# Kernel optimization log

Hardware: AMD Instinct MI355X
Metric: run time of the kernel (lower is better)

Reference implementation:

```python
import jax, jax.numpy as jnp
import numpy as np

# pywt db2 decomposition filters
DEC_LO = np.array([-0.12940952255092145, 0.22414386804185735,
                   0.836516303737469, 0.48296291314469025], dtype=np.float32)
DEC_HI = np.array([-0.48296291314469025, 0.836516303737469,
                   -0.22414386804185735, -0.12940952255092145], dtype=np.float32)

# pywt WaveletPacket2D.get_level(2, order='freq') graycode order over per-axis
# band paths: ['ll','lh','hh','hl'] -> (band at level1, band at level2), 0=low,1=high
GRAY = [(0, 0), (0, 1), (1, 1), (1, 0)]


def _pdwt_last(x, filts):
    """Single-level periodization-mode DWT along last axis.
    pywt 'per' mode (even N): out[i] = sum_j f[j] * x[(2i+1-j) mod N].
    Equivalent to circular left-pad by L-2 then VALID strided conv with the
    time-reversed filter. filts: [2, L] already reversed (lo, hi).
    Returns [..., 2, N//2] (band axis inserted before halved axis)."""
    *lead, N = x.shape
    L = filts.shape[-1]
    xe = jnp.concatenate([x[..., N - (L - 2):], x], axis=-1)  # [..., N+L-2]
    y = jax.lax.conv_general_dilated(
        xe.reshape(-1, 1, N + L - 2), filts[:, None, :],
        window_strides=(2,), padding='VALID')  # [B, 2, N//2]
    return y.reshape(*lead, 2, N // 2)


def _dwt2(x, filts):
    """2D single-level periodized DWT on the last two axes.
    x: [..., H, W] -> [..., 2(row band), 2(col band), H/2, W/2].
    Row band 1 = high-pass along axis -2 (pywt 'h' node = cH = 'da')."""
    y = _pdwt_last(x.swapaxes(-1, -2), filts)      # [..., W, 2, H/2]
    y = jnp.moveaxis(y, -2, -3).swapaxes(-1, -2)   # [..., 2, H/2, W]
    z = _pdwt_last(y, filts)                       # [..., 2, H/2, 2, W/2]
    return jnp.moveaxis(z, -2, -3)                 # [..., 2, 2, H/2, W/2]


def setup_inputs() -> dict:
    key = jax.random.key(0)
    x = jax.random.uniform(key, (3, 2048, 2048), dtype=jnp.float32)  # CHW in [0,1]
    return {"x": x, "dec_lo": jnp.asarray(DEC_LO), "dec_hi": jnp.asarray(DEC_HI)}


def reference(x, dec_lo, dec_hi):
    filts = jnp.stack([dec_lo[::-1], dec_hi[::-1]])  # time-reversed lo/hi, [2, L]
    b1 = _dwt2(x, filts)    # [C, 2, 2, H/2, W/2]            (r1, c1)
    b2 = _dwt2(b1, filts)   # [C, 2, 2, 2, 2, H/4, W/4]      (r1, c1, r2, c2)
    C = x.shape[0]
    h, w = b2.shape[-2:]
    # frequency-ordered 4x4 grid, flattened row-major, channels outermost
    bands = [b2[:, r1, c1, r2, c2] for (r1, r2) in GRAY for (c1, c2) in GRAY]
    y = jnp.stack(bands, axis=1)  # [C, 16, H/4, W/4]
    return y.reshape(C * 16, h, w)
```

## Files before the change

### kernel.cpp

```cpp
#include <hip/hip_runtime.h>

#define HH 2048
#define WW 2048
#define CC 3
#define OH 512
#define OW 512
#define TKC 32
#define TKR 8
#define ROWS 38
#define PITCHF 144
#define V4PR 36
#define NV4 (ROWS * V4PR)
#define NBLK 768
#define TPB 4
#define CTILES 16
#define PERCH 1024

__device__ __forceinline__ float rfl(float v) {
    return __int_as_float(__builtin_amdgcn_readfirstlane(__float_as_int(v)));
}

__global__ __launch_bounds__(256, 3)
void wpt2_kernel(const float* __restrict__ x,
                 const float* __restrict__ dec_lo,
                 const float* __restrict__ dec_hi,
                 float* __restrict__ out) {
    __shared__ float bufA[NV4 * 4];
    __shared__ float bufB[NV4 * 4];

    const int tx  = threadIdx.x;
    const int ty  = threadIdx.y;
    const int tid = ty * TKC + tx;

    const int bid = blockIdx.x;
    const int swz = (bid & 7) * (NBLK / 8) + (bid >> 3);
    const int tile0 = swz * TPB;

    float lo[4], hi[4];
#pragma unroll
    for (int j = 0; j < 4; ++j) { lo[j] = dec_lo[j]; hi[j] = dec_hi[j]; }
    float F[4][10];
#pragma unroll
    for (int g = 0; g < 4; ++g) {
        const float* f1 = (g >= 2) ? hi : lo;
        const float* f2 = (g == 1 || g == 2) ? hi : lo;
#pragma unroll
        for (int d = 0; d < 10; ++d) F[g][d] = 0.f;
#pragma unroll
        for (int j2 = 0; j2 < 4; ++j2)
#pragma unroll
            for (int j1 = 0; j1 < 4; ++j1)
                F[g][2 * j2 + j1] = fmaf(f2[j2], f1[j1], F[g][2 * j2 + j1]);
    }
#pragma unroll
    for (int g = 0; g < 4; ++g)
#pragma unroll
        for (int d = 0; d < 10; ++d) F[g][d] = rfl(F[g][d]);

    auto stage = [&](float* dst, int tileId) {
        const int ch  = tileId >> 10;
        const int rem = tileId & (PERCH - 1);
        const int trr = rem >> 4;
        const int tcc = rem & (CTILES - 1);
        const float* xc = x + (size_t)ch * HH * WW;
        const int r0 = 32 * trr - 6;
        const int c0 = 128 * tcc - 16;
#pragma unroll
        for (int j = 0; j < 6; ++j) {
            const int i = j * 256 + tid;
            if (j < 5 || i < NV4) {
                const int rr = i / V4PR;
                const int vc = i - rr * V4PR;
                int gr = r0 + rr;      if (gr < 0) gr += HH;
                int gc = c0 + 4 * vc;  if (gc < 0) gc += WW;
                __builtin_amdgcn_global_load_lds(
                    (const __attribute__((address_space(1))) void*)&xc[(size_t)gr * WW + gc],
                    (__attribute__((address_space(3))) void*)&dst[i * 4],
                    16, 0, 0);
            }
        }
    };

    auto compute = [&](const float* buf, int tileId) {
        const int ch  = tileId >> 10;
        const int rem = tileId & (PERCH - 1);
        const int trr = rem >> 4;
        const int tcc = rem & (CTILES - 1);

        float t[4][10];
#pragma unroll
        for (int g = 0; g < 4; ++g)
#pragma unroll
            for (int d = 0; d < 10; ++d) t[g][d] = 0.f;

#pragma unroll
        for (int u = 0; u < 10; ++u) {
            const float* rp = &buf[(4 * ty + u) * PITCHF + 4 * tx + 8];
            const float4 a = *reinterpret_cast<const float4*>(rp);
            const float4 b = *reinterpret_cast<const float4*>(rp + 4);
            const float4 c = *reinterpret_cast<const float4*>(rp + 8);
            const float row[12] = {a.x, a.y, a.z, a.w, b.x, b.y, b.z, b.w,
                                   c.x, c.y, c.z, c.w};
            const int dr = 9 - u;
#pragma unroll
            for (int dc = 0; dc < 10; ++dc) {
                const float v = row[11 - dc];
#pragma unroll
                for (int g = 0; g < 4; ++g)
                    t[g][dc] = fmaf(F[g][dr], v, t[g][dc]);
            }
        }

        const int kr = TKR * trr + ty;
        const int kc = TKC * tcc + tx;
        const size_t plane = (size_t)OH * OW;
        const size_t obase = (size_t)(ch * 16) * plane + (size_t)kr * OW + kc;
#pragma unroll
        for (int gi = 0; gi < 4; ++gi) {
#pragma unroll
            for (int gj = 0; gj < 4; ++gj) {
                float acc = 0.f;
#pragma unroll
                for (int dc = 0; dc < 10; ++dc)
                    acc = fmaf(F[gj][dc], t[gi][dc], acc);
                out[obase + (size_t)(gi * 4 + gj) * plane] = acc;
            }
        }
    };

    stage(bufA, tile0);
    __syncthreads();
    stage(bufB, tile0 + 1); compute(bufA, tile0);     __syncthreads();
    stage(bufA, tile0 + 2); compute(bufB, tile0 + 1); __syncthreads();
    stage(bufB, tile0 + 3); compute(bufA, tile0 + 2); __syncthreads();
    compute(bufB, tile0 + 3);
}

extern "C" void kernel_launch(void* const* d_in, const int* in_sizes, int n_in,
                              void* d_out, int out_size, void* d_ws, size_t ws_size,
                              hipStream_t stream) {
    const float* x      = (const float*)d_in[0];
    const float* dec_lo = (const float*)d_in[1];
    const float* dec_hi = (const float*)d_in[2];
    float* out          = (float*)d_out;

    hipLaunchKernelGGL(wpt2_kernel, dim3(NBLK), dim3(TKC, TKR), 0, stream,
                       x, dec_lo, dec_hi, out);
}
```

Measured before the change: 26.67 us.

## Stack block tiles vertically, relax barrier waits, use nontemporal output stores

Each block now processes four vertically adjacent tiles in the same column strip instead of four horizontally consecutive tiles, so the overlapping halo rows are more likely to be reused in cache. The __syncthreads calls are replaced by an explicit s_waitcnt vmcnt(16) plus s_barrier. This waits only for the LDS-bound tile loads and lets the 16 output stores from the previous compute stay in flight across the barrier. Output writes become nontemporal stores to limit cache pollution. The hand-counted vmcnt depends on load and store issue order and on the exact instruction count, which makes it fragile if the code generation changes.

```diff
diff --git a/kernel.cpp b/kernel.cpp
--- a/kernel.cpp
+++ b/kernel.cpp
@@ -2,7 +2,6 @@
 
 #define HH 2048
 #define WW 2048
-#define CC 3
 #define OH 512
 #define OW 512
 #define TKC 32
@@ -13,8 +12,10 @@
 #define NV4 (ROWS * V4PR)
 #define NBLK 768
 #define TPB 4
-#define CTILES 16
-#define PERCH 1024
+
+#define BAR()    __builtin_amdgcn_s_barrier()
+#define SCHED0() __builtin_amdgcn_sched_barrier(0)
+#define WAITV(n) asm volatile("s_waitcnt vmcnt(" #n ")" ::: "memory")
 
 __device__ __forceinline__ float rfl(float v) {
     return __int_as_float(__builtin_amdgcn_readfirstlane(__float_as_int(v)));
@@ -34,7 +35,10 @@
 
     const int bid = blockIdx.x;
     const int swz = (bid & 7) * (NBLK / 8) + (bid >> 3);
-    const int tile0 = swz * TPB;
+    const int ch   = swz >> 8;
+    const int rem  = swz & 255;
+    const int tcc  = rem & 15;
+    const int trr0 = (rem >> 4) * TPB;
 
     float lo[4], hi[4];
 #pragma unroll
@@ -57,12 +61,9 @@
 #pragma unroll
         for (int d = 0; d < 10; ++d) F[g][d] = rfl(F[g][d]);
 
-    auto stage = [&](float* dst, int tileId) {
-        const int ch  = tileId >> 10;
-        const int rem = tileId & (PERCH - 1);
-        const int trr = rem >> 4;
-        const int tcc = rem & (CTILES - 1);
-        const float* xc = x + (size_t)ch * HH * WW;
+    const float* xc = x + (size_t)ch * HH * WW;
+
+    auto stage = [&](float* dst, int trr) {
         const int r0 = 32 * trr - 6;
         const int c0 = 128 * tcc - 16;
 #pragma unroll
@@ -81,12 +82,7 @@
         }
     };
 
-    auto compute = [&](const float* buf, int tileId) {
-        const int ch  = tileId >> 10;
-        const int rem = tileId & (PERCH - 1);
-        const int trr = rem >> 4;
-        const int tcc = rem & (CTILES - 1);
-
+    auto compute = [&](const float* buf, int trr) {
         float t[4][10];
 #pragma unroll
         for (int g = 0; g < 4; ++g)
@@ -114,7 +110,7 @@
         const int kr = TKR * trr + ty;
         const int kc = TKC * tcc + tx;
         const size_t plane = (size_t)OH * OW;
-        const size_t obase = (size_t)(ch * 16) * plane + (size_t)kr * OW + kc;
+        float* op = out + (size_t)(ch * 16) * plane + (size_t)kr * OW + kc;
 #pragma unroll
         for (int gi = 0; gi < 4; ++gi) {
 #pragma unroll
@@ -123,17 +119,20 @@
 #pragma unroll
                 for (int dc = 0; dc < 10; ++dc)
                     acc = fmaf(F[gj][dc], t[gi][dc], acc);
-                out[obase + (size_t)(gi * 4 + gj) * plane] = acc;
+                __builtin_nontemporal_store(acc, op + (size_t)(gi * 4 + gj) * plane);
             }
         }
     };
 
-    stage(bufA, tile0);
-    __syncthreads();
-    stage(bufB, tile0 + 1); compute(bufA, tile0);     __syncthreads();
-    stage(bufA, tile0 + 2); compute(bufB, tile0 + 1); __syncthreads();
-    stage(bufB, tile0 + 3); compute(bufA, tile0 + 2); __syncthreads();
-    compute(bufB, tile0 + 3);
+    stage(bufA, trr0 + 0);
+    WAITV(0);  BAR(); SCHED0();
+    stage(bufB, trr0 + 1); compute(bufA, trr0 + 0);
+    WAITV(16); BAR(); SCHED0();
+    stage(bufA, trr0 + 2); compute(bufB, trr0 + 1);
+    WAITV(16); BAR(); SCHED0();
+    stage(bufB, trr0 + 3); compute(bufA, trr0 + 2);
+    WAITV(16); BAR(); SCHED0();
+    compute(bufB, trr0 + 3);
 }
 
 extern "C" void kernel_launch(void* const* d_in, const int* in_sizes, int n_in,
```

Result: faster. 25.85 us (-3.1%).
